# Kernel optimization log

Measured on AMD Instinct MI355X. Metric: run time of the kernel, lower is better.

The kernel has to match this reference:

```python
import jax, jax.numpy as jnp
import numpy as np

N_NODES = 100000


def gcn_conv(h, W, b, src, dst, n):
    # h: [N, Fin] -> [N, Fout], GCNConv with symmetric normalization + self-loops
    h = h @ W  # transform first (PyG order): [N, Fout]
    loop = jnp.arange(n, dtype=src.dtype)
    src_sl = jnp.concatenate([src, loop])  # [E+N]
    dst_sl = jnp.concatenate([dst, loop])
    deg = jax.ops.segment_sum(jnp.ones_like(dst_sl, dtype=h.dtype), dst_sl, num_segments=n)  # [N]
    dinv = jax.lax.rsqrt(deg)  # deg >= 1 thanks to self-loops
    norm = dinv[src_sl] * dinv[dst_sl]  # [E+N]
    msgs = h[src_sl] * norm[:, None]  # gather + scale: [E+N, Fout]
    out = jax.ops.segment_sum(msgs, dst_sl, num_segments=n)  # scatter-add
    return out + b


def setup_inputs() -> dict:
    key = jax.random.key(0)
    kx, ke, k1, k2 = jax.random.split(key, 4)
    in_dim, hid_dim, out_dim = 512, 128, 40
    x = jax.random.normal(kx, (N_NODES, in_dim), dtype=jnp.float32)
    edge_index = jax.random.randint(ke, (2, 1600000), 0, N_NODES, dtype=jnp.int64)
    s1 = 1.0 / np.sqrt(in_dim)
    s2 = 1.0 / np.sqrt(hid_dim)
    W1 = jax.random.uniform(k1, (in_dim, hid_dim), jnp.float32, -s1, s1)
    b1 = jnp.zeros((hid_dim,), jnp.float32)
    W2 = jax.random.uniform(k2, (hid_dim, out_dim), jnp.float32, -s2, s2)
    b2 = jnp.zeros((out_dim,), jnp.float32)
    return {"x": x, "edge_index": edge_index, "W1": W1, "b1": b1, "W2": W2, "b2": b2}


def reference(x, edge_index, W1, b1, W2, b2):
    src, dst = edge_index[0], edge_index[1]
    n = x.shape[0]
    h = jax.nn.relu(gcn_conv(x, W1, b1, src, dst, n))
    h = gcn_conv(h, W2, b2, src, dst, n)
    return jax.nn.log_softmax(h, axis=1)
```

## Files before the change

### kernel.cpp

```cpp
#include <hip/hip_runtime.h>
#include <math.h>

#define FIN 512
#define FH 128
#define FOUT 40
#define FP 64
#define NB 512
#define PSLOTS 30
#define CAPG 4096
#define PBLK 512

typedef unsigned char u8;
typedef __attribute__((ext_vector_type(8))) short bf16x8;
typedef __attribute__((ext_vector_type(4))) float f32x4;
typedef __attribute__((ext_vector_type(2))) float f32x2;

__device__ inline ushort f2bf(float f){
  union { float f; uint32_t u; } v; v.f = f;
  uint32_t u = v.u;
  uint32_t r = (u + 0x7FFF + ((u >> 16) & 1)) >> 16;
  return (ushort)r;
}
__device__ inline uint32_t cvtpk(float a, float b){
  uint32_t r;
  asm("v_cvt_pk_bf16_f32 %0, %1, %2" : "=v"(r) : "v"(a), "v"(b));
  return r;
}
__device__ inline f32x2 pkadd(f32x2 a, f32x2 b){
  f32x2 r;
  asm("v_pk_add_f32 %0, %1, %2" : "=v"(r) : "v"(a), "v"(b));
  return r;
}
__device__ inline f32x2 f8lo(uint32_t v){ return __builtin_amdgcn_cvt_pk_f32_fp8(v, false); }
__device__ inline f32x2 f8hi(uint32_t v){ return __builtin_amdgcn_cvt_pk_f32_fp8(v, true); }
__device__ inline u8 f2f8(float v){
  return (u8)(__builtin_amdgcn_cvt_pk_fp8_f32(v, v, 0, false) & 0xFF);
}

__global__ __launch_bounds__(256) void k_part(const int* __restrict__ src,
                                              const int* __restrict__ dst, int e,
                                              int* __restrict__ cnt, int* __restrict__ gcur,
                                              uint32_t* __restrict__ gbuf, int n, int npb,
                                              const float* __restrict__ W1,
                                              const float* __restrict__ W2,
                                              ushort* __restrict__ W1t, ushort* __restrict__ W2t){
  __shared__ uint32_t pbuf[NB*PSLOTS];
  __shared__ int lcnt[NB];
  int b = blockIdx.x, t = threadIdx.x;
  int gidx = b*256 + t;
  if(gidx < FIN*FH){
    int k = gidx / FH, c = gidx % FH;
    W1t[(size_t)c*FIN + k] = f2bf(W1[gidx]);
  }
  if(gidx < 48*FH){
    int c = gidx / FH, k = gidx % FH;
    W2t[gidx] = (c < FOUT) ? f2bf(W2[(size_t)k*FOUT + c]) : (ushort)0;
  }
  for(int i=t;i<NB;i+=256) lcnt[i]=0;
  __syncthreads();
  int chunk = (e + PBLK - 1) / PBLK;
  int base = b * chunk;
  int endE = base + chunk; if(endE > e) endE = e;
  if(base >= e) return;
  int rounds = (endE - base + 255) / 256;
  for(int rr=0; rr<rounds; ++rr){
    int i = base + rr*256 + t;
    if(i < endE){
      int s = src[i];
      int d = dst[i];
      atomicAdd(&cnt[d], 1);
      int bk = d / npb;
      uint32_t pk_ = ((uint32_t)s << 8) | (uint32_t)(d - bk*npb);
      int slot = atomicAdd(&lcnt[bk], 1);
      if(slot < PSLOTS){
        pbuf[bk*PSLOTS + slot] = pk_;
      } else {
        int g = atomicAdd(&gcur[bk], 1);
        gbuf[(size_t)bk*CAPG + g] = pk_;
      }
    }
    __syncthreads();
    bool last = (rr == rounds-1);
    for(int tb=t; tb<NB; tb+=256){
      int c = lcnt[tb];
      int k = c < PSLOTS ? c : PSLOTS;
      if(k > 0 && (k >= 16 || last)){
        int g = atomicAdd(&gcur[tb], k);
        uint32_t* dstp = &gbuf[(size_t)tb*CAPG + g];
        const uint32_t* srcp = &pbuf[tb*PSLOTS];
        for(int q=0; q<k; q++) dstp[q] = srcp[q];
        lcnt[tb] = 0;
      }
    }
    __syncthreads();
  }
}

__global__ void k_scan_a(const int* __restrict__ cnt, int n, int* __restrict__ rp, int* __restrict__ aux){
  __shared__ int sh[256];
  int t = threadIdx.x;
  int base = blockIdx.x*1024;
  int v[4]; int s = 0;
  #pragma unroll
  for(int j=0;j<4;j++){ int idx = base + t*4 + j; int x = (idx<n)?cnt[idx]:0; v[j]=x; s+=x; }
  sh[t]=s; __syncthreads();
  for(int off=1; off<256; off<<=1){
    int x = (t>=off)? sh[t-off]:0; __syncthreads();
    sh[t]+=x; __syncthreads();
  }
  int run = (t>0)? sh[t-1]:0;
  #pragma unroll
  for(int j=0;j<4;j++){ run += v[j]; int idx = base + t*4 + j; if(idx<n) rp[idx+1]=run; }
  if(t==255) aux[blockIdx.x]=sh[255];
}

__global__ void k_scan_c(int* __restrict__ rp, const int* __restrict__ aux,
                         const int* __restrict__ cnt, float* __restrict__ dinv,
                         int n, int nchunks){
  __shared__ int sh[256];
  int t = threadIdx.x;
  sh[t] = (t<nchunks)? aux[t] : 0;
  __syncthreads();
  for(int off=1; off<256; off<<=1){
    int x = (t>=off)? sh[t-off]:0; __syncthreads();
    sh[t]+=x; __syncthreads();
  }
  int i = blockIdx.x*256 + t;
  if(i<n){
    int c = i >> 10;
    int add = (c>0)? sh[c-1] : 0;
    rp[i+1] += add;
    dinv[i] = rsqrtf((float)(cnt[i]+1));
  }
  if(i==0) rp[0] = 0;
}

__global__ __launch_bounds__(512, 2) void k_gemm1(const float* __restrict__ X,
                                                  const ushort* __restrict__ W1t,
                                                  const float* __restrict__ dinv,
                                                  u8* __restrict__ XWs, int n){
  __shared__ char smem[65536];
  int t = threadIdx.x;
  int gi = blockIdx.x;
  int lane = t & 63;
  int wid = t >> 6;
  int l15 = lane & 15;
  int lk8 = (lane >> 4) * 8;
  int rowbase = gi * 256 + wid * 32;

  int r0 = rowbase + l15;      if (r0 >= n) r0 = n-1;
  int r1 = rowbase + 16 + l15; if (r1 >= n) r1 = n-1;
  const float* a0p = X + (size_t)r0*FIN;
  const float* a1p = X + (size_t)r1*FIN;

  f32x4 acc[2][8];
  #pragma unroll
  for(int i=0;i<2;i++)
    #pragma unroll
    for(int j=0;j<8;j++) acc[i][j] = (f32x4){0.f,0.f,0.f,0.f};

  char* WsB = smem;

  #pragma unroll
  for(int half=0; half<2; half++){
    if(half) __syncthreads();
    #pragma unroll
    for(int it=0; it<8; it++){
      int c = it*512 + t;
      int col = c >> 5, kslot = c & 31;
      uint4 v = *(const uint4*)(W1t + (size_t)col*FIN + half*256 + kslot*8);
      int dstb = col*512 + ((kslot*16) ^ ((col & 7) << 4));
      *(uint4*)(WsB + dstb) = v;
    }
    __syncthreads();

    for(int kc=0; kc<8; kc++){
      int kl = kc*32 + lk8;
      int kg = half*256 + kl;
      float4 a0a = *(const float4*)(a0p + kg);
      float4 a0b = *(const float4*)(a0p + kg + 4);
      float4 a1a = *(const float4*)(a1p + kg);
      float4 a1b = *(const float4*)(a1p + kg + 4);
      uint4 fa0u, fa1u;
      fa0u.x = cvtpk(a0a.x, a0a.y); fa0u.y = cvtpk(a0a.z, a0a.w);
      fa0u.z = cvtpk(a0b.x, a0b.y); fa0u.w = cvtpk(a0b.z, a0b.w);
      fa1u.x = cvtpk(a1a.x, a1a.y); fa1u.y = cvtpk(a1a.z, a1a.w);
      fa1u.z = cvtpk(a1b.x, a1b.y); fa1u.w = cvtpk(a1b.z, a1b.w);
      bf16x8 fa0 = *(bf16x8*)&fa0u;
      bf16x8 fa1 = *(bf16x8*)&fa1u;

      #pragma unroll
      for(int fj=0; fj<8; fj++){
        int col = fj*16 + l15;
        int srcb = col*512 + ((kl*2) ^ ((col & 7) << 4));
        bf16x8 fb = *(const bf16x8*)(WsB + srcb);
        acc[0][fj] = __builtin_amdgcn_mfma_f32_16x16x32_bf16(fa0, fb, acc[0][fj], 0, 0, 0);
        acc[1][fj] = __builtin_amdgcn_mfma_f32_16x16x32_bf16(fa1, fb, acc[1][fj], 0, 0, 0);
      }
    }
  }

  int rbase = (lane >> 4) * 4;
  #pragma unroll
  for(int fi=0; fi<2; fi++){
    #pragma unroll
    for(int r=0; r<4; r++){
      int row = rowbase + fi*16 + rbase + r;
      if(row < n){
        float dd = dinv[row];
        #pragma unroll
        for(int fj=0; fj<8; fj++){
          XWs[(size_t)row*FH + fj*16 + l15] = f2f8(acc[fi][fj][r] * dd);
        }
      }
    }
  }
}

__global__ __launch_bounds__(512) void k_fill2(const uint32_t* __restrict__ gbuf,
                                               const int* __restrict__ gcur,
                                               const int* __restrict__ rp,
                                               int* __restrict__ srcs, int n, int npb){
  __shared__ int lcur[256];
  int fb = blockIdx.x;
  int t = threadIdx.x;
  int base = fb * npb;
  if(base >= n) return;
  int nn = n - base; if(nn > npb) nn = npb;
  for(int i = t; i < nn; i += 512) lcur[i] = rp[base + i];
  __syncthreads();
  int m = gcur[fb];
  const uint32_t* bp = gbuf + (size_t)fb*CAPG;
  for(int i = t; i < m; i += 512){
    uint32_t v = bp[i];
    int ld = (int)(v & 255u);
    int p = atomicAdd(&lcur[ld], 1);
    srcs[p] = (int)(v >> 8);
  }
}

__global__ __launch_bounds__(256) void k_agg1(const u8* __restrict__ XWs, const int* __restrict__ rp,
                                              const int* __restrict__ srcs, const float* __restrict__ dinv,
                                              const float* __restrict__ b1, ushort* __restrict__ H1b, int n){
  int d = blockIdx.x*4 + (threadIdx.x >> 6);
  if(d >= n) return;
  int lane = threadIdx.x & 63;
  int g = lane >> 3, li = lane & 7;
  f32x2 acc[8];
  #pragma unroll
  for(int k=0;k<8;k++) acc[k] = (f32x2){0.f,0.f};
  int beg = rp[d];
  int end = rp[d+1];
  int j = beg + g;
  bool h0 = j < end, h1 = j + 8 < end;
  int s0 = 0, s1 = 0;
  if(h0) s0 = srcs[j];
  if(h1) s1 = srcs[j+8];
  while(h1){
    int nj = j + 16;
    bool nh0 = nj < end, nh1 = nj + 8 < end;
    int ns0 = 0, ns1 = 0;
    if(nh0) ns0 = srcs[nj];
    if(nh1) ns1 = srcs[nj+8];
    uint4 a0 = *(const uint4*)(XWs + (size_t)s0*FH + li*16);
    uint4 c0 = *(const uint4*)(XWs + (size_t)s1*FH + li*16);
    acc[0] = pkadd(acc[0], pkadd(f8lo(a0.x), f8lo(c0.x)));
    acc[1] = pkadd(acc[1], pkadd(f8hi(a0.x), f8hi(c0.x)));
    acc[2] = pkadd(acc[2], pkadd(f8lo(a0.y), f8lo(c0.y)));
    acc[3] = pkadd(acc[3], pkadd(f8hi(a0.y), f8hi(c0.y)));
    acc[4] = pkadd(acc[4], pkadd(f8lo(a0.z), f8lo(c0.z)));
    acc[5] = pkadd(acc[5], pkadd(f8hi(a0.z), f8hi(c0.z)));
    acc[6] = pkadd(acc[6], pkadd(f8lo(a0.w), f8lo(c0.w)));
    acc[7] = pkadd(acc[7], pkadd(f8hi(a0.w), f8hi(c0.w)));
    j = nj; s0 = ns0; s1 = ns1; h0 = nh0; h1 = nh1;
  }
  if(h0){
    uint4 a0 = *(const uint4*)(XWs + (size_t)s0*FH + li*16);
    acc[0] = pkadd(acc[0], f8lo(a0.x));
    acc[1] = pkadd(acc[1], f8hi(a0.x));
    acc[2] = pkadd(acc[2], f8lo(a0.y));
    acc[3] = pkadd(acc[3], f8hi(a0.y));
    acc[4] = pkadd(acc[4], f8lo(a0.z));
    acc[5] = pkadd(acc[5], f8hi(a0.z));
    acc[6] = pkadd(acc[6], f8lo(a0.w));
    acc[7] = pkadd(acc[7], f8hi(a0.w));
  }
  #pragma unroll
  for(int k=0;k<8;k++){
    #pragma unroll
    for(int c=0;c<2;c++){
      acc[k][c] += __shfl_xor(acc[k][c], 8);
      acc[k][c] += __shfl_xor(acc[k][c], 16);
      acc[k][c] += __shfl_xor(acc[k][c], 32);
    }
  }
  if(g == 0){
    uint4 sv4 = *(const uint4*)(XWs + (size_t)d*FH + li*16);
    f32x2 slf[8];
    slf[0]=f8lo(sv4.x); slf[1]=f8hi(sv4.x); slf[2]=f8lo(sv4.y); slf[3]=f8hi(sv4.y);
    slf[4]=f8lo(sv4.z); slf[5]=f8hi(sv4.z); slf[6]=f8lo(sv4.w); slf[7]=f8hi(sv4.w);
    float dd = dinv[d];
    uint32_t w[8];
    #pragma unroll
    for(int k=0;k<8;k++){
      float b0 = b1[li*16 + k*2];
      float b1v = b1[li*16 + k*2 + 1];
      float o0 = fmaxf((acc[k][0]+slf[k][0])*dd + b0, 0.f);
      float o1 = fmaxf((acc[k][1]+slf[k][1])*dd + b1v, 0.f);
      w[k] = cvtpk(o0, o1);
    }
    uint4 w0 = {w[0],w[1],w[2],w[3]};
    uint4 w1 = {w[4],w[5],w[6],w[7]};
    uint4* wp = (uint4*)(H1b + (size_t)d*FH + li*16);
    wp[0] = w0;
    wp[1] = w1;
  }
}

__global__ __launch_bounds__(256) void k_gemm2_mfma(const ushort* __restrict__ H1b,
                                                    const ushort* __restrict__ W2t,
                                                    const float* __restrict__ dinv,
                                                    u8* __restrict__ H2s, int n){
  int t = threadIdx.x;
  int lane = t & 63;
  int wid = t >> 6;
  int l15 = lane & 15;
  int lk8 = (lane >> 4) * 8;
  int rowbase = blockIdx.x * 128 + wid * 32;

  int r0 = rowbase + l15;      if (r0 >= n) r0 = n-1;
  int r1 = rowbase + 16 + l15; if (r1 >= n) r1 = n-1;
  const ushort* a0p = H1b + (size_t)r0*FH + lk8;
  const ushort* a1p = H1b + (size_t)r1*FH + lk8;

  f32x4 acc[2][3];
  #pragma unroll
  for(int i=0;i<2;i++)
    #pragma unroll
    for(int j=0;j<3;j++) acc[i][j] = (f32x4){0.f,0.f,0.f,0.f};

  #pragma unroll
  for(int kc=0; kc<4; kc++){
    int k0 = kc*32;
    bf16x8 fa0 = *(const bf16x8*)(a0p + k0);
    bf16x8 fa1 = *(const bf16x8*)(a1p + k0);
    #pragma unroll
    for(int fj=0; fj<3; fj++){
      bf16x8 fb = *(const bf16x8*)(W2t + (size_t)(fj*16 + l15)*FH + k0 + lk8);
      acc[0][fj] = __builtin_amdgcn_mfma_f32_16x16x32_bf16(fa0, fb, acc[0][fj], 0, 0, 0);
      acc[1][fj] = __builtin_amdgcn_mfma_f32_16x16x32_bf16(fa1, fb, acc[1][fj], 0, 0, 0);
    }
  }

  int rbase = (lane >> 4) * 4;
  #pragma unroll
  for(int fi=0; fi<2; fi++){
    #pragma unroll
    for(int r=0; r<4; r++){
      int row = rowbase + fi*16 + rbase + r;
      if(row < n){
        float dd = dinv[row];
        #pragma unroll
        for(int fj=0; fj<3; fj++){
          int col = fj*16 + l15;
          H2s[(size_t)row*FP + col] = (col < FOUT) ? f2f8(acc[fi][fj][r] * dd) : (u8)0;
        }
        H2s[(size_t)row*FP + 48 + l15] = (u8)0;
      }
    }
  }
}

__global__ __launch_bounds__(256) void k_agg2_sm(const u8* __restrict__ H2s, const int* __restrict__ rp,
                                                 const int* __restrict__ srcs, const float* __restrict__ dinv,
                                                 const float* __restrict__ b2, float* __restrict__ out, int n){
  int d = blockIdx.x*4 + (threadIdx.x >> 6);
  if(d >= n) return;
  int lane = threadIdx.x & 63;
  int g = lane >> 3, li = lane & 7;
  f32x2 acc[4];
  #pragma unroll
  for(int k=0;k<4;k++) acc[k] = (f32x2){0.f,0.f};
  int beg = rp[d];
  int end = rp[d+1];
  int j = beg + g;
  bool h0 = j < end, h1 = j + 8 < end;
  int s0 = 0, s1 = 0;
  if(h0) s0 = srcs[j];
  if(h1) s1 = srcs[j+8];
  while(h1){
    int nj = j + 16;
    bool nh0 = nj < end, nh1 = nj + 8 < end;
    int ns0 = 0, ns1 = 0;
    if(nh0) ns0 = srcs[nj];
    if(nh1) ns1 = srcs[nj+8];
    uint2 v = *(const uint2*)(H2s + (size_t)s0*FP + li*8);
    uint2 u = *(const uint2*)(H2s + (size_t)s1*FP + li*8);
    acc[0] = pkadd(acc[0], pkadd(f8lo(v.x), f8lo(u.x)));
    acc[1] = pkadd(acc[1], pkadd(f8hi(v.x), f8hi(u.x)));
    acc[2] = pkadd(acc[2], pkadd(f8lo(v.y), f8lo(u.y)));
    acc[3] = pkadd(acc[3], pkadd(f8hi(v.y), f8hi(u.y)));
    j = nj; s0 = ns0; s1 = ns1; h0 = nh0; h1 = nh1;
  }
  if(h0){
    uint2 v = *(const uint2*)(H2s + (size_t)s0*FP + li*8);
    acc[0] = pkadd(acc[0], f8lo(v.x));
    acc[1] = pkadd(acc[1], f8hi(v.x));
    acc[2] = pkadd(acc[2], f8lo(v.y));
    acc[3] = pkadd(acc[3], f8hi(v.y));
  }
  #pragma unroll
  for(int k=0;k<4;k++){
    #pragma unroll
    for(int c=0;c<2;c++){
      acc[k][c] += __shfl_xor(acc[k][c], 8);
      acc[k][c] += __shfl_xor(acc[k][c], 16);
      acc[k][c] += __shfl_xor(acc[k][c], 32);
    }
  }
  uint2 sv = *(const uint2*)(H2s + (size_t)d*FP + li*8);
  f32x2 s2[4] = { f8lo(sv.x), f8hi(sv.x), f8lo(sv.y), f8hi(sv.y) };
  float dd = dinv[d];
  float val[8];
  #pragma unroll
  for(int k=0;k<4;k++){
    #pragma unroll
    for(int c=0;c<2;c++){
      int col = li*8 + k*2 + c;
      float bv = (col < FOUT) ? b2[col] : 0.f;
      val[k*2+c] = (col < FOUT) ? ((acc[k][c]+s2[k][c])*dd + bv) : -3.402823466e38f;
    }
  }
  float m = val[0];
  #pragma unroll
  for(int k=1;k<8;k++) m = fmaxf(m, val[k]);
  #pragma unroll
  for(int off=1; off<8; off<<=1) m = fmaxf(m, __shfl_xor(m, off));
  float ssum = 0.f;
  #pragma unroll
  for(int k=0;k<8;k++){
    int col = li*8 + k;
    ssum += (col < FOUT) ? expf(val[k] - m) : 0.f;
  }
  #pragma unroll
  for(int off=1; off<8; off<<=1) ssum += __shfl_xor(ssum, off);
  float lse = m + logf(ssum);
  if(g == 0 && li < 5){
    float4 o0 = {val[0]-lse, val[1]-lse, val[2]-lse, val[3]-lse};
    float4 o1 = {val[4]-lse, val[5]-lse, val[6]-lse, val[7]-lse};
    float* op = out + (size_t)d*FOUT + li*8;
    *(float4*)op = o0;
    *(float4*)(op+4) = o1;
  }
}


extern "C" void kernel_launch(void* const* d_in, const int* in_sizes, int n_in,
                              void* d_out, int out_size, void* d_ws, size_t ws_size,
                              hipStream_t stream){
  const float* X  = (const float*)d_in[0];
  const int*   ei = (const int*)d_in[1];
  const float* W1 = (const float*)d_in[2];
  const float* b1 = (const float*)d_in[3];
  const float* W2 = (const float*)d_in[4];
  const float* b2 = (const float*)d_in[5];
  float* out = (float*)d_out;

  int n = in_sizes[0] / FIN;
  int e = in_sizes[1] / 2;
  const int* src = ei;
  const int* dst = ei + e;

  int npb = (n + NB - 1) / NB;

  u8* XWs     = (u8*)d_ws;
  ushort* H1b = (ushort*)(XWs + (size_t)n*FH);
  u8* H2s     = (u8*)(H1b + (size_t)n*FH);
  ushort* W1t = (ushort*)(H2s + (size_t)n*FP);
  ushort* W2t = W1t + (size_t)FH*FIN;
  float* dinv = (float*)(W2t + 48*FH);
  int* cnt    = (int*)(dinv + n);
  int* gcur   = cnt + n;
  int* rp     = gcur + NB;
  int* srcs   = rp + (n+1) + 3;
  int* aux    = srcs + e;
  uint32_t* gbuf = (uint32_t*)H1b;

  int nchunks = (n + 1023) / 1024;
  int G = (n + 255) / 256;

  hipMemsetAsync(cnt, 0, (size_t)(n + NB)*sizeof(int), stream);
  hipLaunchKernelGGL(k_part, dim3(PBLK), dim3(256), 0, stream,
                     src, dst, e, cnt, gcur, gbuf, n, npb, W1, W2, W1t, W2t);
  hipLaunchKernelGGL(k_scan_a, dim3(nchunks), dim3(256), 0, stream, cnt, n, rp, aux);
  hipLaunchKernelGGL(k_scan_c, dim3((n+255)/256), dim3(256), 0, stream, rp, aux, cnt, dinv, n, nchunks);

  hipLaunchKernelGGL(k_gemm1, dim3(G), dim3(512), 0, stream, X, W1t, dinv, XWs, n);
  hipLaunchKernelGGL(k_fill2, dim3(NB), dim3(512), 0, stream, gbuf, gcur, rp, srcs, n, npb);

  hipLaunchKernelGGL(k_agg1, dim3((n+3)/4), dim3(256), 0, stream, XWs, rp, srcs, dinv, b1, H1b, n);
  hipLaunchKernelGGL(k_gemm2_mfma, dim3((n+127)/128), dim3(256), 0, stream, H1b, W2t, dinv, H2s, n);
  hipLaunchKernelGGL(k_agg2_sm, dim3((n+3)/4), dim3(256), 0, stream, H2s, rp, srcs, dinv, b2, out, n);
}
```

Baseline: 292.3 us.

## Derive degree histogram from bucketed edges instead of global atomics

After: 247.9 us. 15.2% less time.

```diff
diff --git a/kernel.cpp b/kernel.cpp
--- a/kernel.cpp
+++ b/kernel.cpp
@@ -39,7 +39,7 @@
 
 __global__ __launch_bounds__(256) void k_part(const int* __restrict__ src,
                                               const int* __restrict__ dst, int e,
-                                              int* __restrict__ cnt, int* __restrict__ gcur,
+                                              int* __restrict__ gcur,
                                               uint32_t* __restrict__ gbuf, int n, int npb,
                                               const float* __restrict__ W1,
                                               const float* __restrict__ W2,
@@ -68,7 +68,6 @@
     if(i < endE){
       int s = src[i];
       int d = dst[i];
-      atomicAdd(&cnt[d], 1);
       int bk = d / npb;
       uint32_t pk_ = ((uint32_t)s << 8) | (uint32_t)(d - bk*npb);
       int slot = atomicAdd(&lcnt[bk], 1);
@@ -96,41 +95,51 @@
   }
 }
 
-__global__ void k_scan_a(const int* __restrict__ cnt, int n, int* __restrict__ rp, int* __restrict__ aux){
+__global__ __launch_bounds__(256) void k_hist(const uint32_t* __restrict__ gbuf,
+                                              const int* __restrict__ gcur,
+                                              int* __restrict__ rp, float* __restrict__ dinv,
+                                              int* __restrict__ aux, int n, int npb){
+  __shared__ int hist[256];
   __shared__ int sh[256];
-  int t = threadIdx.x;
-  int base = blockIdx.x*1024;
-  int v[4]; int s = 0;
-  #pragma unroll
-  for(int j=0;j<4;j++){ int idx = base + t*4 + j; int x = (idx<n)?cnt[idx]:0; v[j]=x; s+=x; }
-  sh[t]=s; __syncthreads();
-  for(int off=1; off<256; off<<=1){
-    int x = (t>=off)? sh[t-off]:0; __syncthreads();
-    sh[t]+=x; __syncthreads();
-  }
-  int run = (t>0)? sh[t-1]:0;
-  #pragma unroll
-  for(int j=0;j<4;j++){ run += v[j]; int idx = base + t*4 + j; if(idx<n) rp[idx+1]=run; }
-  if(t==255) aux[blockIdx.x]=sh[255];
-}
-
-__global__ void k_scan_c(int* __restrict__ rp, const int* __restrict__ aux,
-                         const int* __restrict__ cnt, float* __restrict__ dinv,
-                         int n, int nchunks){
-  __shared__ int sh[256];
-  int t = threadIdx.x;
-  sh[t] = (t<nchunks)? aux[t] : 0;
+  int b = blockIdx.x, t = threadIdx.x;
+  int base = b * npb;
+  if(base >= n){ if(t==0) aux[b] = 0; return; }
+  hist[t] = 0;
+  __syncthreads();
+  int m = gcur[b];
+  const uint32_t* bp = gbuf + (size_t)b*CAPG;
+  for(int i=t; i<m; i+=256) atomicAdd(&hist[bp[i] & 255u], 1);
+  __syncthreads();
+  int v = hist[t];
+  sh[t] = v;
   __syncthreads();
   for(int off=1; off<256; off<<=1){
     int x = (t>=off)? sh[t-off]:0; __syncthreads();
     sh[t]+=x; __syncthreads();
   }
-  int i = blockIdx.x*256 + t;
+  int nn = n - base; if(nn > npb) nn = npb;
+  if(t < nn){
+    rp[base+t+1] = sh[t];
+    dinv[base+t] = rsqrtf((float)(v+1));
+  }
+  if(t==255) aux[b] = sh[255];
+}
+
+__global__ __launch_bounds__(512) void k_scan_c(int* __restrict__ rp, const int* __restrict__ aux,
+                                                int n, int npb){
+  __shared__ int sh[512];
+  int t = threadIdx.x;
+  sh[t] = aux[t];
+  __syncthreads();
+  for(int off=1; off<512; off<<=1){
+    int x = (t>=off)? sh[t-off]:0; __syncthreads();
+    sh[t]+=x; __syncthreads();
+  }
+  int i = blockIdx.x*512 + t;
   if(i<n){
-    int c = i >> 10;
-    int add = (c>0)? sh[c-1] : 0;
+    int b = i / npb;
+    int add = (b>0)? sh[b-1] : 0;
     rp[i+1] += add;
-    dinv[i] = rsqrtf((float)(cnt[i]+1));
   }
   if(i==0) rp[0] = 0;
 }
@@ -479,21 +488,19 @@
   ushort* W1t = (ushort*)(H2s + (size_t)n*FP);
   ushort* W2t = W1t + (size_t)FH*FIN;
   float* dinv = (float*)(W2t + 48*FH);
-  int* cnt    = (int*)(dinv + n);
-  int* gcur   = cnt + n;
+  int* gcur   = (int*)(dinv + n);
   int* rp     = gcur + NB;
   int* srcs   = rp + (n+1) + 3;
   int* aux    = srcs + e;
   uint32_t* gbuf = (uint32_t*)H1b;
 
-  int nchunks = (n + 1023) / 1024;
   int G = (n + 255) / 256;
 
-  hipMemsetAsync(cnt, 0, (size_t)(n + NB)*sizeof(int), stream);
+  hipMemsetAsync(gcur, 0, (size_t)NB*sizeof(int), stream);
   hipLaunchKernelGGL(k_part, dim3(PBLK), dim3(256), 0, stream,
-                     src, dst, e, cnt, gcur, gbuf, n, npb, W1, W2, W1t, W2t);
-  hipLaunchKernelGGL(k_scan_a, dim3(nchunks), dim3(256), 0, stream, cnt, n, rp, aux);
-  hipLaunchKernelGGL(k_scan_c, dim3((n+255)/256), dim3(256), 0, stream, rp, aux, cnt, dinv, n, nchunks);
+                     src, dst, e, gcur, gbuf, n, npb, W1, W2, W1t, W2t);
+  hipLaunchKernelGGL(k_hist, dim3(NB), dim3(256), 0, stream, gbuf, gcur, rp, dinv, aux, n, npb);
+  hipLaunchKernelGGL(k_scan_c, dim3((n+511)/512), dim3(512), 0, stream, rp, aux, n, npb);
 
   hipLaunchKernelGGL(k_gemm1, dim3(G), dim3(512), 0, stream, X, W1t, dinv, XWs, n);
   hipLaunchKernelGGL(k_fill2, dim3(NB), dim3(512), 0, stream, gbuf, gcur, rp, srcs, n, npb);
```
